# Performance work log

Hardware: AMD Instinct MI355X
Metric: run time of the kernel (lower is better)

## Reference

```python
import jax, jax.numpy as jnp
import numpy as np

N = 50000
E = 800000
IN = 128
HID = 64
HEADS = 4
OUT = 128
NEG_SLOPE = 0.2


def _segment_softmax(logits, seg, num_segments):
    # logits: (E, H), seg: (E,) destination node ids
    m = jax.ops.segment_max(logits, seg, num_segments=num_segments)
    m = jnp.where(jnp.isfinite(m), m, 0.0)
    e = jnp.exp(logits - m[seg])
    s = jax.ops.segment_sum(e, seg, num_segments=num_segments)
    return e / (s[seg] + 1e-16)


def _gat_conv(x, edge_index, W, att_src, att_dst, bias, heads, out_ch, concat):
    # PyG GATConv with add_self_loops=True, negative_slope=0.2 (eval mode: no dropout)
    n = x.shape[0]
    loops = jnp.arange(n, dtype=edge_index.dtype)
    src = jnp.concatenate([edge_index[0], loops])
    dst = jnp.concatenate([edge_index[1], loops])
    h = (x @ W).reshape(n, heads, out_ch)                      # (N, H, C)
    a_src = jnp.einsum('nhc,hc->nh', h, att_src)               # (N, H)
    a_dst = jnp.einsum('nhc,hc->nh', h, att_dst)
    logits = jax.nn.leaky_relu(a_src[src] + a_dst[dst], NEG_SLOPE)  # (E', H)
    alpha = _segment_softmax(logits, dst, n)                   # (E', H)
    msg = alpha[:, :, None] * h[src]                           # (E', H, C)
    out = jax.ops.segment_sum(msg, dst, num_segments=n)        # (N, H, C)
    if concat:
        out = out.reshape(n, heads * out_ch)
    else:
        out = out.mean(axis=1)
    return out + bias


def setup_inputs() -> dict:
    key = jax.random.key(0)
    ks = jax.random.split(key, 16)
    hc = HID * HEADS
    s = 0.1
    return {
        'x': jax.random.normal(ks[0], (N, IN), dtype=jnp.float32),
        'edge_index': jax.random.randint(ks[1], (2, E), 0, N, dtype=jnp.int64),
        'W1': jax.random.normal(ks[2], (IN, hc), dtype=jnp.float32) * s,
        'att_src1': jax.random.normal(ks[3], (HEADS, HID), dtype=jnp.float32) * s,
        'att_dst1': jax.random.normal(ks[4], (HEADS, HID), dtype=jnp.float32) * s,
        'b1': jnp.zeros((hc,), dtype=jnp.float32),
        'lin1_w': jax.random.normal(ks[5], (IN, hc), dtype=jnp.float32) * s,
        'lin1_b': jnp.zeros((hc,), dtype=jnp.float32),
        'W2': jax.random.normal(ks[6], (hc, OUT), dtype=jnp.float32) * s,
        'att_src2': jax.random.normal(ks[7], (1, OUT), dtype=jnp.float32) * s,
        'att_dst2': jax.random.normal(ks[8], (1, OUT), dtype=jnp.float32) * s,
        'b2': jnp.zeros((OUT,), dtype=jnp.float32),
        'lin2_w': jax.random.normal(ks[9], (hc, OUT), dtype=jnp.float32) * s,
        'lin2_b': jnp.zeros((OUT,), dtype=jnp.float32),
    }


def reference(x, edge_index, W1, att_src1, att_dst1, b1, lin1_w, lin1_b,
              W2, att_src2, att_dst2, b2, lin2_w, lin2_b):
    # h1 = ELU(GATConv1(x) + Linear1(x))  (dropout is eval-mode no-op)
    h = _gat_conv(x, edge_index, W1, att_src1, att_dst1, b1, HEADS, HID, True)
    h = jax.nn.elu(h + x @ lin1_w + lin1_b)
    # out = GATConv2(h) + Linear2(h)
    o = _gat_conv(h, edge_index, W2, att_src2, att_dst2, b2, 1, OUT, False)
    return o + h @ lin2_w + lin2_b
```

## Files before the change

kernel.cpp:

```cpp
#include <hip/hip_runtime.h>
#include <math.h>

#define N_NODES 50000
#define N_EDGES 800000
#define EP (N_EDGES + N_NODES)
#define IN_CH 128
#define HID 64
#define HEADS 4
#define HC (HID * HEADS)
#define OUT_CH 128
#define NEG_SLOPE 0.2f
#define NSCAN ((N_NODES + 255) / 256)
#define MTILES (N_NODES / 16)

typedef __bf16 bf16x8 __attribute__((ext_vector_type(8)));
typedef float  f32x4  __attribute__((ext_vector_type(4)));

__device__ __forceinline__ float bf2f(unsigned short u) {
    return __uint_as_float(((unsigned)u) << 16);
}
__device__ __forceinline__ unsigned short f2bf(float f) {
    unsigned u = __float_as_uint(f);
    return (unsigned short)((u + 0x7fffu + ((u >> 16) & 1u)) >> 16);
}
__device__ __forceinline__ float lrelu(float v) {
    return v > 0.f ? v : NEG_SLOPE * v;
}
__device__ __forceinline__ bf16x8 ldfrag(const unsigned short* p) {
    uint4 u = *(const uint4*)p;
    return __builtin_bit_cast(bf16x8, u);
}

__global__ void hist_kernel(const int* __restrict__ ei, int* __restrict__ cnt) {
    int e = blockIdx.x * 256 + threadIdx.x;
    if (e >= EP) return;
    int d = (e < N_EDGES) ? ei[N_EDGES + e] : e - N_EDGES;
    atomicAdd(&cnt[d], 1);
}

__global__ void scan1_kernel(const int* __restrict__ cnt,
                             int* __restrict__ row, int* __restrict__ bsum) {
    __shared__ int buf[256];
    int i = blockIdx.x * 256 + threadIdx.x;
    int v = (i < N_NODES) ? cnt[i] : 0;
    buf[threadIdx.x] = v;
    __syncthreads();
#pragma unroll
    for (int off = 1; off < 256; off <<= 1) {
        int t = (threadIdx.x >= off) ? buf[threadIdx.x - off] : 0;
        __syncthreads();
        buf[threadIdx.x] += t;
        __syncthreads();
    }
    if (i < N_NODES) row[i] = buf[threadIdx.x] - v;
    if (threadIdx.x == 255) bsum[blockIdx.x] = buf[255];
}

__global__ void scan2_kernel(const int* __restrict__ bsum,
                             int* __restrict__ boff, int* __restrict__ rowN) {
    __shared__ int buf[256];
    int tid = threadIdx.x;
    int v = (tid < NSCAN) ? bsum[tid] : 0;
    buf[tid] = v;
    __syncthreads();
#pragma unroll
    for (int off = 1; off < 256; off <<= 1) {
        int t = (tid >= off) ? buf[tid - off] : 0;
        __syncthreads();
        buf[tid] += t;
        __syncthreads();
    }
    if (tid < NSCAN) boff[tid] = buf[tid] - v;
    if (tid == 255) rowN[0] = buf[255];
}

__global__ void scan3_kernel(int* __restrict__ row, const int* __restrict__ boff,
                             int* __restrict__ pos) {
    int i = blockIdx.x * 256 + threadIdx.x;
    if (i >= N_NODES) return;
    int r = row[i] + boff[blockIdx.x];
    row[i] = r;
    pos[i] = r;
}

__global__ void scatter_el1_kernel(const int* __restrict__ ei,
                                   int* __restrict__ pos,
                                   const float4* __restrict__ AS4,
                                   const float4* __restrict__ AD4,
                                   int* __restrict__ adjS, int* __restrict__ adjD,
                                   float4* __restrict__ EL4) {
    int e = blockIdx.x * 256 + threadIdx.x;
    if (e >= EP) return;
    int s, d;
    if (e < N_EDGES) { s = ei[e]; d = ei[N_EDGES + e]; }
    else             { s = d = e - N_EDGES; }
    int p = atomicAdd(&pos[d], 1);
    adjS[p] = s;
    adjD[p] = d;
    float4 a = AS4[s], b = AD4[d];
    float4 o;
    o.x = expf(lrelu(a.x + b.x));
    o.y = expf(lrelu(a.y + b.y));
    o.z = expf(lrelu(a.z + b.z));
    o.w = expf(lrelu(a.w + b.w));
    EL4[p] = o;
}

__global__ void convx_kernel(const float* __restrict__ x,
                             unsigned short* __restrict__ xb) {
    int i = blockIdx.x * 256 + threadIdx.x;
    if (i >= N_NODES * (IN_CH / 4)) return;
    float4 v = ((const float4*)x)[i];
    ushort4 o;
    o.x = f2bf(v.x); o.y = f2bf(v.y); o.z = f2bf(v.z); o.w = f2bf(v.w);
    ((ushort4*)xb)[i] = o;
}

__global__ void pack12_kernel(const float* __restrict__ W1,
                              const float* __restrict__ L1,
                              const float* __restrict__ W2,
                              const float* __restrict__ L2,
                              unsigned short* __restrict__ Bp1,
                              unsigned short* __restrict__ Bp2) {
    int t = blockIdx.x * 256 + threadIdx.x;
    if (t < 8192) {
        int frag = t >> 6, l = t & 63;
        int ks = frag >> 5, nf = frag & 31;
        int col = nf * 16 + (l & 15);
        int kb = ks * 32 + (l >> 4) * 8;
        unsigned short* o = Bp1 + (size_t)t * 8;
#pragma unroll
        for (int i = 0; i < 8; ++i) {
            int k = kb + i;
            float v = (col < HC) ? W1[k * HC + col] : L1[k * HC + (col - HC)];
            o[i] = f2bf(v);
        }
    } else if (t < 16384) {
        int u = t - 8192;
        int frag = u >> 6, l = u & 63;
        int ks = frag >> 4, nf = frag & 15;
        int col = nf * 16 + (l & 15);
        int kb = ks * 32 + (l >> 4) * 8;
        unsigned short* o = Bp2 + (size_t)u * 8;
#pragma unroll
        for (int i = 0; i < 8; ++i) {
            int k = kb + i;
            float v = (col < OUT_CH) ? W2[k * OUT_CH + col]
                                     : L2[k * OUT_CH + (col - OUT_CH)];
            o[i] = f2bf(v);
        }
    }
}

__global__ __launch_bounds__(256) void gemm1_mfma(
        const unsigned short* __restrict__ xb,
        const unsigned short* __restrict__ Bp,
        const float* __restrict__ as1, const float* __restrict__ ad1,
        unsigned short* __restrict__ H1b, unsigned short* __restrict__ XLb,
        float* __restrict__ AS, float* __restrict__ AD) {
    __shared__ float sAS[16][4], sAD[16][4];
    int m0 = blockIdx.x * 16;
    int w = threadIdx.x >> 6, l = threadIdx.x & 63;
    int arow = m0 + (l & 15);
    int koff = (l >> 4) * 8;
    f32x4 acc[8];
#pragma unroll
    for (int f = 0; f < 8; ++f) acc[f] = (f32x4){0.f, 0.f, 0.f, 0.f};
#pragma unroll
    for (int ks = 0; ks < 4; ++ks) {
        bf16x8 a = ldfrag(xb + (size_t)arow * IN_CH + ks * 32 + koff);
        const unsigned short* bb = Bp + ((size_t)((ks * 32 + w * 8) * 64 + l)) * 8;
#pragma unroll
        for (int f = 0; f < 8; ++f) {
            bf16x8 b = ldfrag(bb + (size_t)f * 512);
            acc[f] = __builtin_amdgcn_mfma_f32_16x16x32_bf16(a, b, acc[f], 0, 0, 0);
        }
    }
    int g = l >> 4, lc = l & 15;
#pragma unroll
    for (int f = 0; f < 8; ++f) {
        int col = w * 128 + f * 16 + lc;
#pragma unroll
        for (int r = 0; r < 4; ++r) {
            int m = m0 + g * 4 + r;
            float v = acc[f][r];
            if (col < HC) H1b[(size_t)m * HC + col] = f2bf(v);
            else          XLb[(size_t)m * HC + (col - HC)] = f2bf(v);
        }
    }
    if (w < 2) {
        float ps[4][2], pd[4][2];
#pragma unroll
        for (int r = 0; r < 4; ++r) { ps[r][0]=ps[r][1]=pd[r][0]=pd[r][1]=0.f; }
#pragma unroll
        for (int f = 0; f < 8; ++f) {
            int col = w * 128 + f * 16 + lc;
            float av = as1[col], dv = ad1[col];
            int hp = f >> 2;
#pragma unroll
            for (int r = 0; r < 4; ++r) {
                ps[r][hp] += acc[f][r] * av;
                pd[r][hp] += acc[f][r] * dv;
            }
        }
#pragma unroll
        for (int msk = 1; msk < 16; msk <<= 1)
#pragma unroll
            for (int r = 0; r < 4; ++r) {
                ps[r][0] += __shfl_xor(ps[r][0], msk, 64);
                ps[r][1] += __shfl_xor(ps[r][1], msk, 64);
                pd[r][0] += __shfl_xor(pd[r][0], msk, 64);
                pd[r][1] += __shfl_xor(pd[r][1], msk, 64);
            }
        if (lc == 0)
#pragma unroll
            for (int r = 0; r < 4; ++r) {
                sAS[g * 4 + r][w * 2 + 0] = ps[r][0];
                sAS[g * 4 + r][w * 2 + 1] = ps[r][1];
                sAD[g * 4 + r][w * 2 + 0] = pd[r][0];
                sAD[g * 4 + r][w * 2 + 1] = pd[r][1];
            }
    }
    __syncthreads();
    int t = threadIdx.x;
    if (t < 64)       AS[(m0 + (t >> 2)) * 4 + (t & 3)] = sAS[t >> 2][t & 3];
    else if (t < 128) { int u = t - 64;
                        AD[(m0 + (u >> 2)) * 4 + (u & 3)] = sAD[u >> 2][u & 3]; }
}

__global__ __launch_bounds__(256) void gemm2_mfma(
        const unsigned short* __restrict__ HBb,
        const unsigned short* __restrict__ Bp,
        const float* __restrict__ as2, const float* __restrict__ ad2,
        unsigned short* __restrict__ H2b, unsigned short* __restrict__ XLb,
        float* __restrict__ AS, float* __restrict__ AD) {
    __shared__ float sAS[16][2], sAD[16][2];
    int m0 = blockIdx.x * 16;
    int w = threadIdx.x >> 6, l = threadIdx.x & 63;
    int arow = m0 + (l & 15);
    int koff = (l >> 4) * 8;
    f32x4 acc[4];
#pragma unroll
    for (int f = 0; f < 4; ++f) acc[f] = (f32x4){0.f, 0.f, 0.f, 0.f};
#pragma unroll
    for (int ks = 0; ks < 8; ++ks) {
        bf16x8 a = ldfrag(HBb + (size_t)arow * HC + ks * 32 + koff);
        const unsigned short* bb = Bp + ((size_t)((ks * 16 + w * 4) * 64 + l)) * 8;
#pragma unroll
        for (int f = 0; f < 4; ++f) {
            bf16x8 b = ldfrag(bb + (size_t)f * 512);
            acc[f] = __builtin_amdgcn_mfma_f32_16x16x32_bf16(a, b, acc[f], 0, 0, 0);
        }
    }
    int g = l >> 4, lc = l & 15;
#pragma unroll
    for (int f = 0; f < 4; ++f) {
        int col = w * 64 + f * 16 + lc;
#pragma unroll
        for (int r = 0; r < 4; ++r) {
            int m = m0 + g * 4 + r;
            float v = acc[f][r];
            if (col < OUT_CH) H2b[(size_t)m * OUT_CH + col] = f2bf(v);
            else              XLb[(size_t)m * OUT_CH + (col - OUT_CH)] = f2bf(v);
        }
    }
    if (w < 2) {
        float ps[4], pd[4];
#pragma unroll
        for (int r = 0; r < 4; ++r) { ps[r] = 0.f; pd[r] = 0.f; }
#pragma unroll
        for (int f = 0; f < 4; ++f) {
            int col = w * 64 + f * 16 + lc;
            float av = as2[col], dv = ad2[col];
#pragma unroll
            for (int r = 0; r < 4; ++r) {
                ps[r] += acc[f][r] * av;
                pd[r] += acc[f][r] * dv;
            }
        }
#pragma unroll
        for (int msk = 1; msk < 16; msk <<= 1)
#pragma unroll
            for (int r = 0; r < 4; ++r) {
                ps[r] += __shfl_xor(ps[r], msk, 64);
                pd[r] += __shfl_xor(pd[r], msk, 64);
            }
        if (lc == 0)
#pragma unroll
            for (int r = 0; r < 4; ++r) {
                sAS[g * 4 + r][w] = ps[r];
                sAD[g * 4 + r][w] = pd[r];
            }
    }
    __syncthreads();
    int t = threadIdx.x;
    if (t < 16)       AS[m0 + t] = sAS[t][0] + sAS[t][1];
    else if (t < 32)  { int u = t - 16; AD[m0 + u] = sAD[u][0] + sAD[u][1]; }
}

__global__ void el2_kernel(const int* __restrict__ adjS,
                           const int* __restrict__ adjD,
                           const float* __restrict__ AS,
                           const float* __restrict__ AD,
                           float* __restrict__ EL) {
    int p = blockIdx.x * 256 + threadIdx.x;
    if (p >= EP) return;
    EL[p] = expf(lrelu(AS[adjS[p]] + AD[adjD[p]]));
}

__global__ void gather1_kernel(const int* __restrict__ row,
                               const int* __restrict__ adjS,
                               const float4* __restrict__ EL4,
                               const unsigned short* __restrict__ H1b,
                               const unsigned short* __restrict__ XLb,
                               const float* __restrict__ b1,
                               const float* __restrict__ l1b,
                               unsigned short* __restrict__ HBb) {
    int d = blockIdx.x, j = threadIdx.x;
    int hh = j >> 4;
    int beg = row[d], end = row[d + 1];
    const ushort4* Hr = (const ushort4*)H1b;
    float a0 = 0.f, a1 = 0.f, a2 = 0.f, a3 = 0.f, esum = 0.f;
    int i = beg;
    for (; i + 8 <= end; i += 8) {
        int sa[8]; float ea[8]; ushort4 qa[8];
#pragma unroll
        for (int k = 0; k < 8; ++k) sa[k] = adjS[i + k];
#pragma unroll
        for (int k = 0; k < 8; ++k) {
            float4 t = EL4[i + k];
            ea[k] = hh < 2 ? (hh == 0 ? t.x : t.y) : (hh == 2 ? t.z : t.w);
        }
#pragma unroll
        for (int k = 0; k < 8; ++k) qa[k] = Hr[(size_t)sa[k] * 64 + j];
#pragma unroll
        for (int k = 0; k < 8; ++k) {
            a0 += ea[k] * bf2f(qa[k].x); a1 += ea[k] * bf2f(qa[k].y);
            a2 += ea[k] * bf2f(qa[k].z); a3 += ea[k] * bf2f(qa[k].w);
            esum += ea[k];
        }
    }
    for (; i < end; ++i) {
        int s = adjS[i];
        float4 t = EL4[i];
        float e = hh < 2 ? (hh == 0 ? t.x : t.y) : (hh == 2 ? t.z : t.w);
        ushort4 q = Hr[(size_t)s * 64 + j];
        a0 += e * bf2f(q.x); a1 += e * bf2f(q.y);
        a2 += e * bf2f(q.z); a3 += e * bf2f(q.w);
        esum += e;
    }
    float inv = 1.f / (esum + 1e-16f);
    ushort4 xq = ((const ushort4*)XLb)[(size_t)d * 64 + j];
    float4 bb = ((const float4*)b1)[j];
    float4 lb = ((const float4*)l1b)[j];
    float v0 = a0 * inv + bf2f(xq.x) + bb.x + lb.x;
    float v1 = a1 * inv + bf2f(xq.y) + bb.y + lb.y;
    float v2 = a2 * inv + bf2f(xq.z) + bb.z + lb.z;
    float v3 = a3 * inv + bf2f(xq.w) + bb.w + lb.w;
    v0 = v0 > 0.f ? v0 : expm1f(v0);
    v1 = v1 > 0.f ? v1 : expm1f(v1);
    v2 = v2 > 0.f ? v2 : expm1f(v2);
    v3 = v3 > 0.f ? v3 : expm1f(v3);
    ushort4 o;
    o.x = f2bf(v0); o.y = f2bf(v1); o.z = f2bf(v2); o.w = f2bf(v3);
    ((ushort4*)HBb)[(size_t)d * 64 + j] = o;
}

__global__ void gather2_kernel(const int* __restrict__ row,
                               const int* __restrict__ adjS,
                               const float* __restrict__ EL,
                               const unsigned short* __restrict__ H2b,
                               const unsigned short* __restrict__ XLb,
                               const float* __restrict__ b2,
                               const float* __restrict__ l2b,
                               float* __restrict__ out) {
    int d = blockIdx.x, l = threadIdx.x;
    int beg = row[d], end = row[d + 1];
    const ushort2* Hr = (const ushort2*)H2b;
    float ax = 0.f, ay = 0.f, esum = 0.f;
    int i = beg;
    for (; i + 8 <= end; i += 8) {
        int sa[8]; float ea[8]; ushort2 qa[8];
#pragma unroll
        for (int k = 0; k < 8; ++k) sa[k] = adjS[i + k];
#pragma unroll
        for (int k = 0; k < 8; ++k) ea[k] = EL[i + k];
#pragma unroll
        for (int k = 0; k < 8; ++k) qa[k] = Hr[(size_t)sa[k] * 64 + l];
#pragma unroll
        for (int k = 0; k < 8; ++k) {
            ax += ea[k] * bf2f(qa[k].x);
            ay += ea[k] * bf2f(qa[k].y);
            esum += ea[k];
        }
    }
    for (; i < end; ++i) {
        int s = adjS[i];
        float e = EL[i];
        ushort2 q = Hr[(size_t)s * 64 + l];
        ax += e * bf2f(q.x); ay += e * bf2f(q.y);
        esum += e;
    }
    float inv = 1.f / (esum + 1e-16f);
    ushort2 xq = ((const ushort2*)XLb)[(size_t)d * 64 + l];
    float2 bb = ((const float2*)b2)[l];
    float2 lb = ((const float2*)l2b)[l];
    ((float2*)out)[(size_t)d * 64 + l] =
        make_float2(ax * inv + bf2f(xq.x) + bb.x + lb.x,
                    ay * inv + bf2f(xq.y) + bb.y + lb.y);
}

extern "C" void kernel_launch(void* const* d_in, const int* in_sizes, int n_in,
                              void* d_out, int out_size, void* d_ws, size_t ws_size,
                              hipStream_t stream) {
    const float* x    = (const float*)d_in[0];
    const int*   ei   = (const int*)d_in[1];
    const float* W1   = (const float*)d_in[2];
    const float* as1  = (const float*)d_in[3];
    const float* ad1  = (const float*)d_in[4];
    const float* b1   = (const float*)d_in[5];
    const float* l1w  = (const float*)d_in[6];
    const float* l1b  = (const float*)d_in[7];
    const float* W2   = (const float*)d_in[8];
    const float* as2  = (const float*)d_in[9];
    const float* ad2  = (const float*)d_in[10];
    const float* b2   = (const float*)d_in[11];
    const float* l2w  = (const float*)d_in[12];
    const float* l2b  = (const float*)d_in[13];
    float* out = (float*)d_out;

    float* ws = (float*)d_ws;
    unsigned short* xb  = (unsigned short*)ws;
    float* fp = ws + (size_t)N_NODES * 64;
    unsigned short* H1b = (unsigned short*)fp;
    fp += (size_t)N_NODES * 128;
    unsigned short* XLb = (unsigned short*)fp;
    fp += (size_t)N_NODES * 128;
    unsigned short* HBb = (unsigned short*)fp;
    fp += (size_t)N_NODES * 128;
    float* AS1 = fp; fp += (size_t)N_NODES * HEADS;
    float* AD1 = fp; fp += (size_t)N_NODES * HEADS;
    float* AS2 = fp; fp += N_NODES;
    float* AD2 = fp; fp += N_NODES;
    float* EL1 = fp; fp += (size_t)EP * 4;
    unsigned short* Bp1 = (unsigned short*)fp; fp += 32768;
    unsigned short* Bp2 = (unsigned short*)fp; fp += 32768;
    int* cnt  = (int*)fp;
    int* row  = cnt + N_NODES;
    int* pos  = row + N_NODES + 1;
    int* bsum = pos + N_NODES;
    int* boff = bsum + NSCAN;
    int* adjS = boff + NSCAN;
    int* adjD = adjS + EP;
    unsigned short* H2b = H1b;
    unsigned short* XL2b = XLb;
    float* EL2 = EL1;

    int nE = (EP + 255) / 256;

    hipMemsetAsync(cnt, 0, N_NODES * 4, stream);
    hist_kernel<<<nE, 256, 0, stream>>>(ei, cnt);
    scan1_kernel<<<NSCAN, 256, 0, stream>>>(cnt, row, bsum);
    scan2_kernel<<<1, 256, 0, stream>>>(bsum, boff, row + N_NODES);
    scan3_kernel<<<NSCAN, 256, 0, stream>>>(row, boff, pos);

    convx_kernel<<<(N_NODES * (IN_CH / 4) + 255) / 256, 256, 0, stream>>>(x, xb);
    pack12_kernel<<<64, 256, 0, stream>>>(W1, l1w, W2, l2w, Bp1, Bp2);

    gemm1_mfma<<<MTILES, 256, 0, stream>>>(xb, Bp1, as1, ad1, H1b, XLb, AS1, AD1);
    scatter_el1_kernel<<<nE, 256, 0, stream>>>(ei, pos, (const float4*)AS1,
                                               (const float4*)AD1, adjS, adjD,
                                               (float4*)EL1);
    gather1_kernel<<<N_NODES, 64, 0, stream>>>(row, adjS, (const float4*)EL1,
                                               H1b, XLb, b1, l1b, HBb);

    gemm2_mfma<<<MTILES, 256, 0, stream>>>(HBb, Bp2, as2, ad2, H2b, XL2b, AS2, AD2);
    el2_kernel<<<nE, 256, 0, stream>>>(adjS, adjD, AS2, AD2, EL2);
    gather2_kernel<<<N_NODES, 64, 0, stream>>>(row, adjS, EL2, H2b, XL2b,
                                               b2, l2b, out);
}
```

Before: 280.0 us.

## Fuse fp32-to-bf16 conversion into gemm1 and split gather edges across two waves

Drops the separate convx kernel: gemm1 now loads fp32 x directly and packs bf16 fragments in registers, saving a kernel launch and an extra pass over x. Both gather kernels now use two wavefronts per destination node, each summing half of the edge list, and the halves are combined through shared memory. This raises memory-level parallelism for the ~17-edge average degree, at the cost of a block barrier, doubled thread count, and shorter unrolled loops per wave.

```diff
diff --git a/kernel.cpp b/kernel.cpp
--- a/kernel.cpp
+++ b/kernel.cpp
@@ -15,6 +15,7 @@
 
 typedef __bf16 bf16x8 __attribute__((ext_vector_type(8)));
 typedef float  f32x4  __attribute__((ext_vector_type(4)));
+typedef unsigned short u16x8 __attribute__((ext_vector_type(8)));
 
 __device__ __forceinline__ float bf2f(unsigned short u) {
     return __uint_as_float(((unsigned)u) << 16);
@@ -29,6 +30,12 @@
 __device__ __forceinline__ bf16x8 ldfrag(const unsigned short* p) {
     uint4 u = *(const uint4*)p;
     return __builtin_bit_cast(bf16x8, u);
+}
+__device__ __forceinline__ bf16x8 packA(float4 v0, float4 v1) {
+    u16x8 t;
+    t[0] = f2bf(v0.x); t[1] = f2bf(v0.y); t[2] = f2bf(v0.z); t[3] = f2bf(v0.w);
+    t[4] = f2bf(v1.x); t[5] = f2bf(v1.y); t[6] = f2bf(v1.z); t[7] = f2bf(v1.w);
+    return __builtin_bit_cast(bf16x8, t);
 }
 
 __global__ void hist_kernel(const int* __restrict__ ei, int* __restrict__ cnt) {
@@ -106,16 +113,6 @@
     EL4[p] = o;
 }
 
-__global__ void convx_kernel(const float* __restrict__ x,
-                             unsigned short* __restrict__ xb) {
-    int i = blockIdx.x * 256 + threadIdx.x;
-    if (i >= N_NODES * (IN_CH / 4)) return;
-    float4 v = ((const float4*)x)[i];
-    ushort4 o;
-    o.x = f2bf(v.x); o.y = f2bf(v.y); o.z = f2bf(v.z); o.w = f2bf(v.w);
-    ((ushort4*)xb)[i] = o;
-}
-
 __global__ void pack12_kernel(const float* __restrict__ W1,
                               const float* __restrict__ L1,
                               const float* __restrict__ W2,
@@ -153,7 +150,7 @@
 }
 
 __global__ __launch_bounds__(256) void gemm1_mfma(
-        const unsigned short* __restrict__ xb,
+        const float* __restrict__ x,
         const unsigned short* __restrict__ Bp,
         const float* __restrict__ as1, const float* __restrict__ ad1,
         unsigned short* __restrict__ H1b, unsigned short* __restrict__ XLb,
@@ -163,12 +160,15 @@
     int w = threadIdx.x >> 6, l = threadIdx.x & 63;
     int arow = m0 + (l & 15);
     int koff = (l >> 4) * 8;
+    const float* xrow = x + (size_t)arow * IN_CH + koff;
     f32x4 acc[8];
 #pragma unroll
     for (int f = 0; f < 8; ++f) acc[f] = (f32x4){0.f, 0.f, 0.f, 0.f};
 #pragma unroll
     for (int ks = 0; ks < 4; ++ks) {
-        bf16x8 a = ldfrag(xb + (size_t)arow * IN_CH + ks * 32 + koff);
+        float4 v0 = *(const float4*)(xrow + ks * 32);
+        float4 v1 = *(const float4*)(xrow + ks * 32 + 4);
+        bf16x8 a = packA(v0, v1);
         const unsigned short* bb = Bp + ((size_t)((ks * 32 + w * 8) * 64 + l)) * 8;
 #pragma unroll
         for (int f = 0; f < 8; ++f) {
@@ -308,21 +308,26 @@
     EL[p] = expf(lrelu(AS[adjS[p]] + AD[adjD[p]]));
 }
 
-__global__ void gather1_kernel(const int* __restrict__ row,
-                               const int* __restrict__ adjS,
-                               const float4* __restrict__ EL4,
-                               const unsigned short* __restrict__ H1b,
-                               const unsigned short* __restrict__ XLb,
-                               const float* __restrict__ b1,
-                               const float* __restrict__ l1b,
-                               unsigned short* __restrict__ HBb) {
-    int d = blockIdx.x, j = threadIdx.x;
+__global__ __launch_bounds__(128) void gather1_kernel(
+        const int* __restrict__ row,
+        const int* __restrict__ adjS,
+        const float4* __restrict__ EL4,
+        const unsigned short* __restrict__ H1b,
+        const unsigned short* __restrict__ XLb,
+        const float* __restrict__ b1,
+        const float* __restrict__ l1b,
+        unsigned short* __restrict__ HBb) {
+    __shared__ float part[5][64];
+    int d = blockIdx.x;
+    int w = threadIdx.x >> 6, j = threadIdx.x & 63;
     int hh = j >> 4;
     int beg = row[d], end = row[d + 1];
+    int half = (end - beg + 1) >> 1;
+    int i  = (w == 0) ? beg : beg + half;
+    int ie = (w == 0) ? beg + half : end;
     const ushort4* Hr = (const ushort4*)H1b;
     float a0 = 0.f, a1 = 0.f, a2 = 0.f, a3 = 0.f, esum = 0.f;
-    int i = beg;
-    for (; i + 8 <= end; i += 8) {
+    for (; i + 8 <= ie; i += 8) {
         int sa[8]; float ea[8]; ushort4 qa[8];
 #pragma unroll
         for (int k = 0; k < 8; ++k) sa[k] = adjS[i + k];
@@ -340,7 +345,7 @@
             esum += ea[k];
         }
     }
-    for (; i < end; ++i) {
+    for (; i < ie; ++i) {
         int s = adjS[i];
         float4 t = EL4[i];
         float e = hh < 2 ? (hh == 0 ? t.x : t.y) : (hh == 2 ? t.z : t.w);
@@ -349,6 +354,14 @@
         a2 += e * bf2f(q.z); a3 += e * bf2f(q.w);
         esum += e;
     }
+    if (w == 1) {
+        part[0][j] = a0; part[1][j] = a1; part[2][j] = a2; part[3][j] = a3;
+        part[4][j] = esum;
+    }
+    __syncthreads();
+    if (w == 1) return;
+    a0 += part[0][j]; a1 += part[1][j]; a2 += part[2][j]; a3 += part[3][j];
+    esum += part[4][j];
     float inv = 1.f / (esum + 1e-16f);
     ushort4 xq = ((const ushort4*)XLb)[(size_t)d * 64 + j];
     float4 bb = ((const float4*)b1)[j];
@@ -366,20 +379,25 @@
     ((ushort4*)HBb)[(size_t)d * 64 + j] = o;
 }
 
-__global__ void gather2_kernel(const int* __restrict__ row,
-                               const int* __restrict__ adjS,
-                               const float* __restrict__ EL,
-                               const unsigned short* __restrict__ H2b,
-                               const unsigned short* __restrict__ XLb,
-                               const float* __restrict__ b2,
-                               const float* __restrict__ l2b,
-                               float* __restrict__ out) {
-    int d = blockIdx.x, l = threadIdx.x;
+__global__ __launch_bounds__(128) void gather2_kernel(
+        const int* __restrict__ row,
+        const int* __restrict__ adjS,
+        const float* __restrict__ EL,
+        const unsigned short* __restrict__ H2b,
+        const unsigned short* __restrict__ XLb,
+        const float* __restrict__ b2,
+        const float* __restrict__ l2b,
+        float* __restrict__ out) {
+    __shared__ float part[3][64];
+    int d = blockIdx.x;
+    int w = threadIdx.x >> 6, l = threadIdx.x & 63;
     int beg = row[d], end = row[d + 1];
+    int half = (end - beg + 1) >> 1;
+    int i  = (w == 0) ? beg : beg + half;
+    int ie = (w == 0) ? beg + half : end;
     const ushort2* Hr = (const ushort2*)H2b;
     float ax = 0.f, ay = 0.f, esum = 0.f;
-    int i = beg;
-    for (; i + 8 <= end; i += 8) {
+    for (; i + 8 <= ie; i += 8) {
         int sa[8]; float ea[8]; ushort2 qa[8];
 #pragma unroll
         for (int k = 0; k < 8; ++k) sa[k] = adjS[i + k];
@@ -394,13 +412,19 @@
             esum += ea[k];
         }
     }
-    for (; i < end; ++i) {
+    for (; i < ie; ++i) {
         int s = adjS[i];
         float e = EL[i];
         ushort2 q = Hr[(size_t)s * 64 + l];
         ax += e * bf2f(q.x); ay += e * bf2f(q.y);
         esum += e;
     }
+    if (w == 1) {
+        part[0][l] = ax; part[1][l] = ay; part[2][l] = esum;
+    }
+    __syncthreads();
+    if (w == 1) return;
+    ax += part[0][l]; ay += part[1][l]; esum += part[2][l];
     float inv = 1.f / (esum + 1e-16f);
     ushort2 xq = ((const ushort2*)XLb)[(size_t)d * 64 + l];
     float2 bb = ((const float2*)b2)[l];
@@ -430,8 +454,7 @@
     float* out = (float*)d_out;
 
     float* ws = (float*)d_ws;
-    unsigned short* xb  = (unsigned short*)ws;
-    float* fp = ws + (size_t)N_NODES * 64;
+    float* fp = ws;
     unsigned short* H1b = (unsigned short*)fp;
     fp += (size_t)N_NODES * 128;
     unsigned short* XLb = (unsigned short*)fp;
@@ -464,18 +487,17 @@
     scan2_kernel<<<1, 256, 0, stream>>>(bsum, boff, row + N_NODES);
     scan3_kernel<<<NSCAN, 256, 0, stream>>>(row, boff, pos);
 
-    convx_kernel<<<(N_NODES * (IN_CH / 4) + 255) / 256, 256, 0, stream>>>(x, xb);
     pack12_kernel<<<64, 256, 0, stream>>>(W1, l1w, W2, l2w, Bp1, Bp2);
 
-    gemm1_mfma<<<MTILES, 256, 0, stream>>>(xb, Bp1, as1, ad1, H1b, XLb, AS1, AD1);
+    gemm1_mfma<<<MTILES, 256, 0, stream>>>(x, Bp1, as1, ad1, H1b, XLb, AS1, AD1);
     scatter_el1_kernel<<<nE, 256, 0, stream>>>(ei, pos, (const float4*)AS1,
                                                (const float4*)AD1, adjS, adjD,
                                                (float4*)EL1);
-    gather1_kernel<<<N_NODES, 64, 0, stream>>>(row, adjS, (const float4*)EL1,
-                                               H1b, XLb, b1, l1b, HBb);
+    gather1_kernel<<<N_NODES, 128, 0, stream>>>(row, adjS, (const float4*)EL1,
+                                                H1b, XLb, b1, l1b, HBb);
 
     gemm2_mfma<<<MTILES, 256, 0, stream>>>(HBb, Bp2, as2, ad2, H2b, XL2b, AS2, AD2);
     el2_kernel<<<nE, 256, 0, stream>>>(adjS, adjD, AS2, AD2, EL2);
-    gather2_kernel<<<N_NODES, 64, 0, stream>>>(row, adjS, EL2, H2b, XL2b,
-                                               b2, l2b, out);
-}
+    gather2_kernel<<<N_NODES, 128, 0, stream>>>(row, adjS, EL2, H2b, XL2b,
+                                                b2, l2b, out);
+}
```

Result: slower. 346.0 us (+23.6%).

## Fuse x bf16 conversion into gemm1 and use 32-row tiles staged in LDS

Applied to the files above, without the earlier changes.

Removes the standalone fp32-to-bf16 conversion kernel for x: gemm1 now reads fp32 rows itself, converts them and stages them in padded shared memory. Both GEMMs now process 32 rows per block as two 16-row MFMA tiles, so each B fragment loaded from global memory feeds two MFMAs. gemm2 also stages its A rows through LDS. The aim is to cut one kernel launch, one round trip of x through global memory, and half of the B-fragment traffic. In exchange it uses more registers and LDS and needs bounds checks for the partial last tile.

```diff
diff --git a/kernel.cpp b/kernel.cpp
--- a/kernel.cpp
+++ b/kernel.cpp
@@ -11,7 +11,7 @@
 #define OUT_CH 128
 #define NEG_SLOPE 0.2f
 #define NSCAN ((N_NODES + 255) / 256)
-#define MTILES (N_NODES / 16)
+#define MT32 ((N_NODES + 31) / 32)
 
 typedef __bf16 bf16x8 __attribute__((ext_vector_type(8)));
 typedef float  f32x4  __attribute__((ext_vector_type(4)));
@@ -106,16 +106,6 @@
     EL4[p] = o;
 }
 
-__global__ void convx_kernel(const float* __restrict__ x,
-                             unsigned short* __restrict__ xb) {
-    int i = blockIdx.x * 256 + threadIdx.x;
-    if (i >= N_NODES * (IN_CH / 4)) return;
-    float4 v = ((const float4*)x)[i];
-    ushort4 o;
-    o.x = f2bf(v.x); o.y = f2bf(v.y); o.z = f2bf(v.z); o.w = f2bf(v.w);
-    ((ushort4*)xb)[i] = o;
-}
-
 __global__ void pack12_kernel(const float* __restrict__ W1,
                               const float* __restrict__ L1,
                               const float* __restrict__ W2,
@@ -153,79 +143,148 @@
 }
 
 __global__ __launch_bounds__(256) void gemm1_mfma(
-        const unsigned short* __restrict__ xb,
+        const float* __restrict__ x,
         const unsigned short* __restrict__ Bp,
         const float* __restrict__ as1, const float* __restrict__ ad1,
         unsigned short* __restrict__ H1b, unsigned short* __restrict__ XLb,
         float* __restrict__ AS, float* __restrict__ AD) {
-    __shared__ float sAS[16][4], sAD[16][4];
-    int m0 = blockIdx.x * 16;
-    int w = threadIdx.x >> 6, l = threadIdx.x & 63;
-    int arow = m0 + (l & 15);
-    int koff = (l >> 4) * 8;
-    f32x4 acc[8];
-#pragma unroll
-    for (int f = 0; f < 8; ++f) acc[f] = (f32x4){0.f, 0.f, 0.f, 0.f};
+    __shared__ unsigned short xs[32][136];
+    __shared__ float shAS[32][4], shAD[32][4];
+    int m0 = blockIdx.x * 32;
+    int tid = threadIdx.x;
+    {
+        int srow = tid >> 3, cg = (tid & 7) * 16;
+        int grow = m0 + srow;
+        ushort4 o0 = {0,0,0,0}, o1 = {0,0,0,0}, o2 = {0,0,0,0}, o3 = {0,0,0,0};
+        if (grow < N_NODES) {
+            const float4* src = (const float4*)(x + (size_t)grow * IN_CH + cg);
+            float4 v0 = src[0], v1 = src[1], v2 = src[2], v3 = src[3];
+            o0 = make_ushort4(f2bf(v0.x), f2bf(v0.y), f2bf(v0.z), f2bf(v0.w));
+            o1 = make_ushort4(f2bf(v1.x), f2bf(v1.y), f2bf(v1.z), f2bf(v1.w));
+            o2 = make_ushort4(f2bf(v2.x), f2bf(v2.y), f2bf(v2.z), f2bf(v2.w));
+            o3 = make_ushort4(f2bf(v3.x), f2bf(v3.y), f2bf(v3.z), f2bf(v3.w));
+        }
+        *(ushort4*)&xs[srow][cg + 0]  = o0;
+        *(ushort4*)&xs[srow][cg + 4]  = o1;
+        *(ushort4*)&xs[srow][cg + 8]  = o2;
+        *(ushort4*)&xs[srow][cg + 12] = o3;
+    }
+    __syncthreads();
+    int w = tid >> 6, l = tid & 63;
+    int lc = l & 15, g = l >> 4;
+    f32x4 acc0[8], acc1[8];
+#pragma unroll
+    for (int f = 0; f < 8; ++f) {
+        acc0[f] = (f32x4){0.f, 0.f, 0.f, 0.f};
+        acc1[f] = (f32x4){0.f, 0.f, 0.f, 0.f};
+    }
 #pragma unroll
     for (int ks = 0; ks < 4; ++ks) {
-        bf16x8 a = ldfrag(xb + (size_t)arow * IN_CH + ks * 32 + koff);
+        bf16x8 a0 = ldfrag(&xs[lc][ks * 32 + g * 8]);
+        bf16x8 a1 = ldfrag(&xs[16 + lc][ks * 32 + g * 8]);
         const unsigned short* bb = Bp + ((size_t)((ks * 32 + w * 8) * 64 + l)) * 8;
 #pragma unroll
         for (int f = 0; f < 8; ++f) {
             bf16x8 b = ldfrag(bb + (size_t)f * 512);
-            acc[f] = __builtin_amdgcn_mfma_f32_16x16x32_bf16(a, b, acc[f], 0, 0, 0);
-        }
-    }
-    int g = l >> 4, lc = l & 15;
+            acc0[f] = __builtin_amdgcn_mfma_f32_16x16x32_bf16(a0, b, acc0[f], 0, 0, 0);
+            acc1[f] = __builtin_amdgcn_mfma_f32_16x16x32_bf16(a1, b, acc1[f], 0, 0, 0);
+        }
+    }
 #pragma unroll
     for (int f = 0; f < 8; ++f) {
         int col = w * 128 + f * 16 + lc;
 #pragma unroll
         for (int r = 0; r < 4; ++r) {
             int m = m0 + g * 4 + r;
-            float v = acc[f][r];
+            float v = acc0[f][r];
             if (col < HC) H1b[(size_t)m * HC + col] = f2bf(v);
             else          XLb[(size_t)m * HC + (col - HC)] = f2bf(v);
+            int m2 = m0 + 16 + g * 4 + r;
+            if (m2 < N_NODES) {
+                float v2 = acc1[f][r];
+                if (col < HC) H1b[(size_t)m2 * HC + col] = f2bf(v2);
+                else          XLb[(size_t)m2 * HC + (col - HC)] = f2bf(v2);
+            }
         }
     }
     if (w < 2) {
-        float ps[4][2], pd[4][2];
-#pragma unroll
-        for (int r = 0; r < 4; ++r) { ps[r][0]=ps[r][1]=pd[r][0]=pd[r][1]=0.f; }
-#pragma unroll
-        for (int f = 0; f < 8; ++f) {
-            int col = w * 128 + f * 16 + lc;
-            float av = as1[col], dv = ad1[col];
-            int hp = f >> 2;
-#pragma unroll
-            for (int r = 0; r < 4; ++r) {
-                ps[r][hp] += acc[f][r] * av;
-                pd[r][hp] += acc[f][r] * dv;
+        {
+            float ps[4][2], pd[4][2];
+#pragma unroll
+            for (int r = 0; r < 4; ++r) { ps[r][0]=ps[r][1]=pd[r][0]=pd[r][1]=0.f; }
+#pragma unroll
+            for (int f = 0; f < 8; ++f) {
+                int col = w * 128 + f * 16 + lc;
+                float av = as1[col], dv = ad1[col];
+                int hp = f >> 2;
+#pragma unroll
+                for (int r = 0; r < 4; ++r) {
+                    ps[r][hp] += acc0[f][r] * av;
+                    pd[r][hp] += acc0[f][r] * dv;
+                }
             }
-        }
-#pragma unroll
-        for (int msk = 1; msk < 16; msk <<= 1)
-#pragma unroll
-            for (int r = 0; r < 4; ++r) {
-                ps[r][0] += __shfl_xor(ps[r][0], msk, 64);
-                ps[r][1] += __shfl_xor(ps[r][1], msk, 64);
-                pd[r][0] += __shfl_xor(pd[r][0], msk, 64);
-                pd[r][1] += __shfl_xor(pd[r][1], msk, 64);
+#pragma unroll
+            for (int msk = 1; msk < 16; msk <<= 1)
+#pragma unroll
+                for (int r = 0; r < 4; ++r) {
+                    ps[r][0] += __shfl_xor(ps[r][0], msk, 64);
+                    ps[r][1] += __shfl_xor(ps[r][1], msk, 64);
+                    pd[r][0] += __shfl_xor(pd[r][0], msk, 64);
+                    pd[r][1] += __shfl_xor(pd[r][1], msk, 64);
+                }
+            if (lc == 0)
+#pragma unroll
+                for (int r = 0; r < 4; ++r) {
+                    shAS[g * 4 + r][w * 2 + 0] = ps[r][0];
+                    shAS[g * 4 + r][w * 2 + 1] = ps[r][1];
+                    shAD[g * 4 + r][w * 2 + 0] = pd[r][0];
+                    shAD[g * 4 + r][w * 2 + 1] = pd[r][1];
+                }
+        }
+        {
+            float ps[4][2], pd[4][2];
+#pragma unroll
+            for (int r = 0; r < 4; ++r) { ps[r][0]=ps[r][1]=pd[r][0]=pd[r][1]=0.f; }
+#pragma unroll
+            for (int f = 0; f < 8; ++f) {
+                int col = w * 128 + f * 16 + lc;
+                float av = as1[col], dv = ad1[col];
+                int hp = f >> 2;
+#pragma unroll
+                for (int r = 0; r < 4; ++r) {
+                    ps[r][hp] += acc1[f][r] * av;
+                    pd[r][hp] += acc1[f][r] * dv;
+                }
             }
-        if (lc == 0)
-#pragma unroll
-            for (int r = 0; r < 4; ++r) {
-                sAS[g * 4 + r][w * 2 + 0] = ps[r][0];
-                sAS[g * 4 + r][w * 2 + 1] = ps[r][1];
-                sAD[g * 4 + r][w * 2 + 0] = pd[r][0];
-                sAD[g * 4 + r][w * 2 + 1] = pd[r][1];
-            }
+#pragma unroll
+            for (int msk = 1; msk < 16; msk <<= 1)
+#pragma unroll
+                for (int r = 0; r < 4; ++r) {
+                    ps[r][0] += __shfl_xor(ps[r][0], msk, 64);
+                    ps[r][1] += __shfl_xor(ps[r][1], msk, 64);
+                    pd[r][0] += __shfl_xor(pd[r][0], msk, 64);
+                    pd[r][1] += __shfl_xor(pd[r][1], msk, 64);
+                }
+            if (lc == 0)
+#pragma unroll
+                for (int r = 0; r < 4; ++r) {
+                    shAS[16 + g * 4 + r][w * 2 + 0] = ps[r][0];
+                    shAS[16 + g * 4 + r][w * 2 + 1] = ps[r][1];
+                    shAD[16 + g * 4 + r][w * 2 + 0] = pd[r][0];
+                    shAD[16 + g * 4 + r][w * 2 + 1] = pd[r][1];
+                }
+        }
     }
     __syncthreads();
-    int t = threadIdx.x;
-    if (t < 64)       AS[(m0 + (t >> 2)) * 4 + (t & 3)] = sAS[t >> 2][t & 3];
-    else if (t < 128) { int u = t - 64;
-                        AD[(m0 + (u >> 2)) * 4 + (u & 3)] = sAD[u >> 2][u & 3]; }
+    if (tid < 128) {
+        int rr = tid >> 2, hd = tid & 3;
+        int m = m0 + rr;
+        if (m < N_NODES) AS[m * 4 + hd] = shAS[rr][hd];
+    } else {
+        int u = tid - 128, rr = u >> 2, hd = u & 3;
+        int m = m0 + rr;
+        if (m < N_NODES) AD[m * 4 + hd] = shAD[rr][hd];
+    }
 }
 
 __global__ __launch_bounds__(256) void gemm2_mfma(
@@ -234,68 +293,138 @@
         const float* __restrict__ as2, const float* __restrict__ ad2,
         unsigned short* __restrict__ H2b, unsigned short* __restrict__ XLb,
         float* __restrict__ AS, float* __restrict__ AD) {
-    __shared__ float sAS[16][2], sAD[16][2];
-    int m0 = blockIdx.x * 16;
-    int w = threadIdx.x >> 6, l = threadIdx.x & 63;
-    int arow = m0 + (l & 15);
-    int koff = (l >> 4) * 8;
-    f32x4 acc[4];
-#pragma unroll
-    for (int f = 0; f < 4; ++f) acc[f] = (f32x4){0.f, 0.f, 0.f, 0.f};
+    __shared__ unsigned short hs[32][264];
+    __shared__ float shAS[32][2], shAD[32][2];
+    int m0 = blockIdx.x * 32;
+    int tid = threadIdx.x;
+    {
+        int srow = tid >> 3, cg = (tid & 7) * 32;
+        int grow = m0 + srow;
+        ushort4 z = {0,0,0,0};
+        ushort4 q0 = z, q1 = z, q2 = z, q3 = z;
+        if (grow < N_NODES) {
+            const ushort4* src = (const ushort4*)(HBb + (size_t)grow * HC + cg);
+            q0 = src[0]; q1 = src[1]; q2 = src[2]; q3 = src[3];
+        }
+        *(ushort4*)&hs[srow][cg + 0]  = q0;
+        *(ushort4*)&hs[srow][cg + 4]  = q1;
+        *(ushort4*)&hs[srow][cg + 8]  = q2;
+        *(ushort4*)&hs[srow][cg + 12] = q3;
+        ushort4 q4 = z, q5 = z, q6 = z, q7 = z;
+        if (grow < N_NODES) {
+            const ushort4* src = (const ushort4*)(HBb + (size_t)grow * HC + cg + 16);
+            q4 = src[0]; q5 = src[1]; q6 = src[2]; q7 = src[3];
+        }
+        *(ushort4*)&hs[srow][cg + 16] = q4;
+        *(ushort4*)&hs[srow][cg + 20] = q5;
+        *(ushort4*)&hs[srow][cg + 24] = q6;
+        *(ushort4*)&hs[srow][cg + 28] = q7;
+    }
+    __syncthreads();
+    int w = tid >> 6, l = tid & 63;
+    int lc = l & 15, g = l >> 4;
+    f32x4 acc0[4], acc1[4];
+#pragma unroll
+    for (int f = 0; f < 4; ++f) {
+        acc0[f] = (f32x4){0.f, 0.f, 0.f, 0.f};
+        acc1[f] = (f32x4){0.f, 0.f, 0.f, 0.f};
+    }
 #pragma unroll
     for (int ks = 0; ks < 8; ++ks) {
-        bf16x8 a = ldfrag(HBb + (size_t)arow * HC + ks * 32 + koff);
+        bf16x8 a0 = ldfrag(&hs[lc][ks * 32 + g * 8]);
+        bf16x8 a1 = ldfrag(&hs[16 + lc][ks * 32 + g * 8]);
         const unsigned short* bb = Bp + ((size_t)((ks * 16 + w * 4) * 64 + l)) * 8;
 #pragma unroll
         for (int f = 0; f < 4; ++f) {
             bf16x8 b = ldfrag(bb + (size_t)f * 512);
-            acc[f] = __builtin_amdgcn_mfma_f32_16x16x32_bf16(a, b, acc[f], 0, 0, 0);
-        }
-    }
-    int g = l >> 4, lc = l & 15;
+            acc0[f] = __builtin_amdgcn_mfma_f32_16x16x32_bf16(a0, b, acc0[f], 0, 0, 0);
+            acc1[f] = __builtin_amdgcn_mfma_f32_16x16x32_bf16(a1, b, acc1[f], 0, 0, 0);
+        }
+    }
 #pragma unroll
     for (int f = 0; f < 4; ++f) {
         int col = w * 64 + f * 16 + lc;
 #pragma unroll
         for (int r = 0; r < 4; ++r) {
             int m = m0 + g * 4 + r;
-            float v = acc[f][r];
+            float v = acc0[f][r];
             if (col < OUT_CH) H2b[(size_t)m * OUT_CH + col] = f2bf(v);
             else              XLb[(size_t)m * OUT_CH + (col - OUT_CH)] = f2bf(v);
+            int m2 = m0 + 16 + g * 4 + r;
+            if (m2 < N_NODES) {
+                float v2 = acc1[f][r];
+                if (col < OUT_CH) H2b[(size_t)m2 * OUT_CH + col] = f2bf(v2);
+                else              XLb[(size_t)m2 * OUT_CH + (col - OUT_CH)] = f2bf(v2);
+            }
         }
     }
     if (w < 2) {
-        float ps[4], pd[4];
-#pragma unroll
-        for (int r = 0; r < 4; ++r) { ps[r] = 0.f; pd[r] = 0.f; }
-#pragma unroll
-        for (int f = 0; f < 4; ++f) {
-            int col = w * 64 + f * 16 + lc;
-            float av = as2[col], dv = ad2[col];
-#pragma unroll
-            for (int r = 0; r < 4; ++r) {
-                ps[r] += acc[f][r] * av;
-                pd[r] += acc[f][r] * dv;
+        {
+            float ps[4], pd[4];
+#pragma unroll
+            for (int r = 0; r < 4; ++r) { ps[r] = 0.f; pd[r] = 0.f; }
+#pragma unroll
+            for (int f = 0; f < 4; ++f) {
+                int col = w * 64 + f * 16 + lc;
+                float av = as2[col], dv = ad2[col];
+#pragma unroll
+                for (int r = 0; r < 4; ++r) {
+                    ps[r] += acc0[f][r] * av;
+                    pd[r] += acc0[f][r] * dv;
+                }
             }
-        }
-#pragma unroll
-        for (int msk = 1; msk < 16; msk <<= 1)
-#pragma unroll
-            for (int r = 0; r < 4; ++r) {
-                ps[r] += __shfl_xor(ps[r], msk, 64);
-                pd[r] += __shfl_xor(pd[r], msk, 64);
+#pragma unroll
+            for (int msk = 1; msk < 16; msk <<= 1)
+#pragma unroll
+                for (int r = 0; r < 4; ++r) {
+                    ps[r] += __shfl_xor(ps[r], msk, 64);
+                    pd[r] += __shfl_xor(pd[r], msk, 64);
+                }
+            if (lc == 0)
+#pragma unroll
+                for (int r = 0; r < 4; ++r) {
+                    shAS[g * 4 + r][w] = ps[r];
+                    shAD[g * 4 + r][w] = pd[r];
+                }
+        }
+        {
+            float ps[4], pd[4];
+#pragma unroll
+            for (int r = 0; r < 4; ++r) { ps[r] = 0.f; pd[r] = 0.f; }
+#pragma unroll
+            for (int f = 0; f < 4; ++f) {
+                int col = w * 64 + f * 16 + lc;
+                float av = as2[col], dv = ad2[col];
+#pragma unroll
+                for (int r = 0; r < 4; ++r) {
+                    ps[r] += acc1[f][r] * av;
+                    pd[r] += acc1[f][r] * dv;
+                }
             }
-        if (lc == 0)
-#pragma unroll
-            for (int r = 0; r < 4; ++r) {
-                sAS[g * 4 + r][w] = ps[r];
-                sAD[g * 4 + r][w] = pd[r];
-            }
+#pragma unroll
+            for (int msk = 1; msk < 16; msk <<= 1)
+#pragma unroll
+                for (int r = 0; r < 4; ++r) {
+                    ps[r] += __shfl_xor(ps[r], msk, 64);
+                    pd[r] += __shfl_xor(pd[r], msk, 64);
+                }
+            if (lc == 0)
+#pragma unroll
+                for (int r = 0; r < 4; ++r) {
+                    shAS[16 + g * 4 + r][w] = ps[r];
+                    shAD[16 + g * 4 + r][w] = pd[r];
+                }
+        }
     }
     __syncthreads();
-    int t = threadIdx.x;
-    if (t < 16)       AS[m0 + t] = sAS[t][0] + sAS[t][1];
-    else if (t < 32)  { int u = t - 16; AD[m0 + u] = sAD[u][0] + sAD[u][1]; }
+    if (tid < 32) {
+        int m = m0 + tid;
+        if (m < N_NODES) AS[m] = shAS[tid][0] + shAS[tid][1];
+    } else if (tid < 64) {
+        int u = tid - 32;
+        int m = m0 + u;
+        if (m < N_NODES) AD[m] = shAD[u][0] + shAD[u][1];
+    }
 }
 
 __global__ void el2_kernel(const int* __restrict__ adjS,
@@ -430,8 +559,7 @@
     float* out = (float*)d_out;
 
     float* ws = (float*)d_ws;
-    unsigned short* xb  = (unsigned short*)ws;
-    float* fp = ws + (size_t)N_NODES * 64;
+    float* fp = ws;
     unsigned short* H1b = (unsigned short*)fp;
     fp += (size_t)N_NODES * 128;
     unsigned short* XLb = (unsigned short*)fp;
@@ -464,17 +592,16 @@
     scan2_kernel<<<1, 256, 0, stream>>>(bsum, boff, row + N_NODES);
     scan3_kernel<<<NSCAN, 256, 0, stream>>>(row, boff, pos);
 
-    convx_kernel<<<(N_NODES * (IN_CH / 4) + 255) / 256, 256, 0, stream>>>(x, xb);
     pack12_kernel<<<64, 256, 0, stream>>>(W1, l1w, W2, l2w, Bp1, Bp2);
 
-    gemm1_mfma<<<MTILES, 256, 0, stream>>>(xb, Bp1, as1, ad1, H1b, XLb, AS1, AD1);
+    gemm1_mfma<<<MT32, 256, 0, stream>>>(x, Bp1, as1, ad1, H1b, XLb, AS1, AD1);
     scatter_el1_kernel<<<nE, 256, 0, stream>>>(ei, pos, (const float4*)AS1,
                                                (const float4*)AD1, adjS, adjD,
                                                (float4*)EL1);
     gather1_kernel<<<N_NODES, 64, 0, stream>>>(row, adjS, (const float4*)EL1,
                                                H1b, XLb, b1, l1b, HBb);
 
-    gemm2_mfma<<<MTILES, 256, 0, stream>>>(HBb, Bp2, as2, ad2, H2b, XL2b, AS2, AD2);
+    gemm2_mfma<<<MT32, 256, 0, stream>>>(HBb, Bp2, as2, ad2, H2b, XL2b, AS2, AD2);
     el2_kernel<<<nE, 256, 0, stream>>>(adjS, adjD, AS2, AD2, EL2);
     gather2_kernel<<<N_NODES, 64, 0, stream>>>(row, adjS, EL2, H2b, XL2b,
                                                b2, l2b, out);
```

New measurement: 270.2 us (median of 2 runs). 3.5% less time.
